# Performance work log

Measured on AMD Instinct MI355X. Metric: run time of the kernel, lower is better.

## Reference

```python
import jax, jax.numpy as jnp
import numpy as np

N, S, D, H, E, ETYPES = 1024, 64, 256, 4, 4096, 4
HD = D // H
EPS = 1e-5


def setup_inputs() -> dict:
    key = jax.random.key(0)
    ks = jax.random.split(key, 8)
    node_features = jax.random.normal(ks[0], (N, S, D), dtype=jnp.float32)
    lengths = jax.random.randint(ks[1], (N,), 1, S + 1)
    node_masks = (jnp.arange(S)[None, :] < lengths[:, None]).astype(jnp.float32)
    # unique edges (torch builds an adjacency matrix, so duplicates collapse)
    rng = np.random.default_rng(0)
    cand = rng.integers(0, N, size=(4 * E, 2))
    uniq = np.unique(cand, axis=0)
    assert uniq.shape[0] >= E
    perm = rng.permutation(uniq.shape[0])[:E]
    edge_index = jnp.asarray(uniq[perm].T, dtype=jnp.int64)  # [2, E]
    edge_type = jnp.asarray(rng.integers(1, ETYPES + 1, size=(E,)), dtype=jnp.int64)
    scale = 0.02
    wq = jax.random.normal(ks[2], (D, D), jnp.float32) * scale
    wk = jax.random.normal(ks[3], (D, D), jnp.float32) * scale
    wv = jax.random.normal(ks[4], (D, D), jnp.float32) * scale
    wo = jax.random.normal(ks[5], (D, D), jnp.float32) * scale
    return dict(
        node_features=node_features, node_masks=node_masks,
        ln_w=jnp.ones((D,), jnp.float32), ln_b=jnp.zeros((D,), jnp.float32),
        wq=wq, bq=jnp.zeros((D,), jnp.float32),
        wk=wk, bk=jnp.zeros((D,), jnp.float32),
        wv=wv, bv=jnp.zeros((D,), jnp.float32),
        wo=wo, bo=jnp.zeros((D,), jnp.float32),
        edge_type_weights=jnp.ones((ETYPES,), jnp.float32),
        edge_index=edge_index, edge_type=edge_type,
    )


def reference(node_features, node_masks, ln_w, ln_b, wq, bq, wk, bk, wv, bv,
              wo, bo, edge_type_weights, edge_index, edge_type):
    n, s, d = node_features.shape
    # LayerNorm (biased variance, eps=1e-5, as torch)
    mu = jnp.mean(node_features, axis=-1, keepdims=True)
    var = jnp.mean((node_features - mu) ** 2, axis=-1, keepdims=True)
    xn = (node_features - mu) * jax.lax.rsqrt(var + EPS) * ln_w + ln_b
    q = (xn @ wq + bq).reshape(n, s, H, HD)
    k = (xn @ wk + bk).reshape(n, s, H, HD)
    v = (xn @ wv + bv).reshape(n, s, H, HD)
    src, dst = edge_index[0], edge_index[1]
    # per-edge scalar bias: softplus(edge_type_weights[type-1]).clamp(1e-6, 1e6)
    ew = jnp.clip(jax.nn.softplus(edge_type_weights[edge_type - 1]), 1e-6, 1e6)  # [E]
    qe, ke, ve = q[src], k[dst], v[dst]              # [E,S,H,HD]
    km = node_masks[dst]                              # [E,S] key-side mask
    qm = node_masks[src]                              # [E,S] query-side mask
    scores = jnp.einsum('eqhd,ekhd->ehqk', qe, ke) / jnp.sqrt(jnp.float32(HD))
    scores = scores + ew[:, None, None, None]
    neg = jnp.float32(-1e30)
    scores = jnp.where(km[:, None, None, :] > 0, scores, neg)
    # per-edge softmax over the key node's valid tokens; zero rows where no valid key
    attn = jax.nn.softmax(scores, axis=-1) * km[:, None, None, :]
    ctx = jnp.einsum('ehqk,ekhd->eqhd', attn, ve) * qm[:, :, None, None]  # [E,S,H,HD]
    out = jax.ops.segment_sum(ctx, src, num_segments=n)   # sum over incident edges
    out = out.reshape(n, s, d)
    out = out @ wo + bo                                   # output projection (dropout=eval noop)
    out = out + node_features                             # residual
    return out * node_masks[..., None]
```

## Files before the change

kernel.cpp:

```cpp
#include <hip/hip_runtime.h>

#define DDIM 256
#define NEDGE 4096
#define SLEN 64
#define NNODE 1024
#define ROWS 65536

typedef short s16x8 __attribute__((ext_vector_type(8)));
typedef float f32x4 __attribute__((ext_vector_type(4)));

static __device__ __forceinline__ unsigned short f2bf(float f){
  union { float f; unsigned u; } v; v.f = f;
  unsigned r = v.u + 0x7FFFu + ((v.u >> 16) & 1u);
  return (unsigned short)(r >> 16);
}

static __device__ __forceinline__ void gl2lds16(const unsigned short* g, unsigned short* l){
  __builtin_amdgcn_global_load_lds((const __attribute__((address_space(1))) unsigned int*)g,
                                   (__attribute__((address_space(3))) unsigned int*)l, 16, 0, 0);
}

__global__ __launch_bounds__(256) void setup_kernel(const float* nf, const float* lnw, const float* lnb,
                                                    const float* wq, const float* wk, const float* wv, const float* wo,
                                                    const float* bq, const float* bk, const float* bv,
                                                    const float* masks, const int* eidx,
                                                    unsigned short* xn, unsigned short* Wqkv, unsigned short* Wo_t,
                                                    float* qkvb, int* lenp, int* deg){
  int bid = blockIdx.x, tid = threadIdx.x;
  if (bid < 16384){
    int lane = tid & 63;
    int row = bid*4 + (tid >> 6);
    const float4 x4 = ((const float4*)(nf + (size_t)row*DDIM))[lane];
    float s  = x4.x + x4.y + x4.z + x4.w;
    float sq = x4.x*x4.x + x4.y*x4.y + x4.z*x4.z + x4.w*x4.w;
    for (int off=1; off<64; off<<=1){ s += __shfl_xor(s, off); sq += __shfl_xor(sq, off); }
    float mu  = s  * (1.0f/DDIM);
    float var = sq * (1.0f/DDIM) - mu*mu;
    float rs  = rsqrtf(var + 1e-5f);
    float4 w4 = ((const float4*)lnw)[lane];
    float4 b4 = ((const float4*)lnb)[lane];
    ushort4 o;
    o.x = f2bf((x4.x - mu)*rs*w4.x + b4.x);
    o.y = f2bf((x4.y - mu)*rs*w4.y + b4.y);
    o.z = f2bf((x4.z - mu)*rs*w4.z + b4.z);
    o.w = f2bf((x4.w - mu)*rs*w4.w + b4.w);
    ((ushort4*)(xn + (size_t)row*DDIM))[lane] = o;
  } else if (bid < 17412){
    int idx = (bid - 16384)*256 + tid;
    if (idx < 196608){
      int mat = idx >> 16;
      int rem = idx & 65535;
      int n = rem >> 8, k = rem & 255;
      const float* W = (mat==0)?wq:(mat==1)?wk:wv;
      Wqkv[(size_t)(mat*256 + n)*256 + k] = f2bf(W[k*256 + n]);
    } else if (idx < 262144){
      int rem = idx - 196608;
      int n = rem >> 8, k = rem & 255;
      Wo_t[(size_t)n*256 + k] = f2bf(wo[k*256 + n]);
    } else if (idx < 262912){
      int i = idx - 262144;
      qkvb[i] = (i < 256) ? bq[i] : (i < 512) ? bk[i-256] : bv[i-512];
    }
  } else if (bid < 17668){
    int lane = tid & 63;
    int node = (bid - 17412)*4 + (tid >> 6);
    unsigned long long b = __ballot(masks[node*SLEN + lane] > 0.f);
    if (lane == 0) lenp[node] = __popcll(b);
  } else {
    int e = (bid - 17668)*256 + tid;
    if (e < NEDGE) atomicAdd(&deg[eidx[e]], 1);
  }
}

__global__ void scan_kernel(const int* deg, int* startp, int* order){
  __shared__ int buf[NNODE];
  __shared__ int hist[65];
  int t = threadIdx.x;
  int d = deg[t];
  buf[t] = d;
  if (t < 65) hist[t] = 0;
  __syncthreads();
  for (int off=1; off<NNODE; off<<=1){
    int v = (t >= off) ? buf[t-off] : 0;
    __syncthreads();
    buf[t] += v;
    __syncthreads();
  }
  startp[t] = buf[t] - d;
  int dc = d > 64 ? 64 : d;
  atomicAdd(&hist[dc], 1);
  __syncthreads();
  if (t == 0){
    int acc = 0;
    for (int i = 64; i >= 0; i--){ int h = hist[i]; hist[i] = acc; acc += h; }
  }
  __syncthreads();
  int pos = atomicAdd(&hist[dc], 1);
  order[pos] = t;
}

__global__ __launch_bounds__(256) void edge_fill_kernel(const int* eidx, const int* startp, int* cursor, int* elist){
  int e = blockIdx.x*256 + threadIdx.x;
  if (e < NEDGE){
    int s = eidx[e];
    int p = atomicAdd(&cursor[s], 1);
    elist[startp[s] + p] = eidx[NEDGE + e];
  }
}

__global__ __launch_bounds__(256) void qkv_kernel(const unsigned short* xn, const unsigned short* Wqkv,
                                                  const float* qkvb,
                                                  unsigned short* qb, unsigned short* kb_, unsigned short* vt){
  __shared__ __align__(16) unsigned short As[4096];
  __shared__ __align__(16) unsigned short Bs[8192];
  int tid = threadIdx.x;
  int lane = tid & 63, wid = tid >> 6, m = lane & 15, quad = lane >> 4;
  int row0 = blockIdx.x * 64;
  int col0 = blockIdx.y * 128;
  int rw = (wid & 1) * 32, cw = (wid >> 1) * 64;
  f32x4 acc[8];
  #pragma unroll
  for (int i=0;i<8;i++) acc[i] = (f32x4){0.f,0.f,0.f,0.f};
  for (int kc = 0; kc < 4; kc++){
    __syncthreads();
    #pragma unroll
    for (int i=0;i<2;i++){
      int cid = i*256 + tid, row = cid >> 3, c8 = cid & 7;
      gl2lds16(xn + (size_t)(row0 + row)*DDIM + kc*64 + ((c8 ^ (row&7))<<3), As + cid*8);
    }
    #pragma unroll
    for (int i=0;i<4;i++){
      int cid = i*256 + tid, row = cid >> 3, c8 = cid & 7;
      gl2lds16(Wqkv + (size_t)(col0 + row)*DDIM + kc*64 + ((c8 ^ (row&7))<<3), Bs + cid*8);
    }
    __syncthreads();
    #pragma unroll
    for (int ks=0; ks<2; ks++){
      int sw = ((ks*4 + quad) ^ (m&7)) << 3;
      s16x8 af[2], bf[4];
      #pragma unroll
      for (int mt=0;mt<2;mt++) af[mt] = *(const s16x8*)(As + (rw + mt*16 + m)*64 + sw);
      #pragma unroll
      for (int nt=0;nt<4;nt++) bf[nt] = *(const s16x8*)(Bs + (cw + nt*16 + m)*64 + sw);
      #pragma unroll
      for (int mt=0;mt<2;mt++)
        #pragma unroll
        for (int nt=0;nt<4;nt++)
          acc[mt*4+nt] = __builtin_amdgcn_mfma_f32_16x16x32_bf16(af[mt], bf[nt], acc[mt*4+nt], 0,0,0);
    }
  }
  int node = row0 >> 6;
  #pragma unroll
  for (int nt=0;nt<4;nt++){
    int cg = col0 + cw + nt*16 + m;
    int mat = cg >> 8, col = cg & 255;
    float bb = qkvb[cg];
    if (mat < 2){
      unsigned short* ob = (mat==0)?qb:kb_;
      #pragma unroll
      for (int mt=0;mt<2;mt++)
        #pragma unroll
        for (int r=0;r<4;r++){
          int row = row0 + rw + mt*16 + quad*4 + r;
          ob[(size_t)row*DDIM + col] = f2bf(acc[mt*4+nt][r] + bb);
        }
    } else {
      #pragma unroll
      for (int mt=0;mt<2;mt++){
        int tok0 = rw + mt*16 + quad*4;
        ushort4 p;
        p.x = f2bf(acc[mt*4+nt][0] + bb);
        p.y = f2bf(acc[mt*4+nt][1] + bb);
        p.z = f2bf(acc[mt*4+nt][2] + bb);
        p.w = f2bf(acc[mt*4+nt][3] + bb);
        *(ushort4*)(vt + ((size_t)node*256 + col)*64 + tok0) = p;
      }
    }
  }
}

__global__ __launch_bounds__(256) void attn_kernel(const unsigned short* qb, const unsigned short* kbuf,
                                                   const unsigned short* vtb, const int* lenp,
                                                   const int* startp, const int* degp, const int* elist,
                                                   const int* order, unsigned short* ctxb){
  __shared__ __align__(16) unsigned short Kt[2][4096];
  __shared__ __align__(16) unsigned short Vt[2][4096];
  __shared__ unsigned short P[4096];
  int tid = threadIdx.x;
  int lane = tid & 63, wid = tid >> 6, m = lane & 15, quad = lane >> 4;
  int src = order[blockIdx.x], h = blockIdx.y;
  int ls = lenp[src];
  int qtm = (ls + 15) >> 4;
  int s0 = startp[src], dg = degp[src];
  bool active = wid < qtm;
  unsigned short* Pw = P + wid*1024;

  s16x8 qf0 = {0,0,0,0,0,0,0,0}, qf1 = {0,0,0,0,0,0,0,0};
  if (active){
    const unsigned short* qbase = qb + (size_t)(src*SLEN + wid*16 + m)*DDIM + h*64 + quad*8;
    qf0 = *(const s16x8*)(qbase);
    qf1 = *(const s16x8*)(qbase + 32);
  }
  f32x4 o[4];
  #pragma unroll
  for (int i=0;i<4;i++) o[i] = (f32x4){0.f,0.f,0.f,0.f};

  int dst0 = 0, dst1 = 0, ld0 = 0;
  if (dg > 0){
    dst0 = elist[s0];
    ld0 = lenp[dst0];
    int kch = ((ld0 + 15) >> 4) * 128;
    #pragma unroll
    for (int i=0;i<2;i++){
      int cid = i*256 + tid;
      if (i*256 + wid*64 < kch){
        int row = cid >> 3, c8 = cid & 7;
        gl2lds16(kbuf + (size_t)(dst0*SLEN + row)*DDIM + h*64 + ((c8 ^ (row&7))<<3), Kt[0] + cid*8);
      }
    }
    const unsigned short* vhead = vtb + ((size_t)dst0*256 + h*64)*64;
    #pragma unroll
    for (int i=0;i<2;i++){
      int cid = i*256 + tid, row = cid >> 3, c8 = cid & 7;
      gl2lds16(vhead + row*64 + ((c8 ^ (row&7))<<3), Vt[0] + cid*8);
    }
  }
  if (dg > 1) dst1 = elist[s0 + 1];
  __syncthreads();

  for (int ei=0; ei<dg; ei++){
    int cur = ei & 1, nxt = cur ^ 1;
    int dst2 = (ei+2 < dg) ? elist[s0 + ei + 2] : 0;
    int ld1 = 0;
    if (ei+1 < dg){
      ld1 = lenp[dst1];
      int kch = ((ld1 + 15) >> 4) * 128;
      #pragma unroll
      for (int i=0;i<2;i++){
        int cid = i*256 + tid;
        if (i*256 + wid*64 < kch){
          int row = cid >> 3, c8 = cid & 7;
          gl2lds16(kbuf + (size_t)(dst1*SLEN + row)*DDIM + h*64 + ((c8 ^ (row&7))<<3), Kt[nxt] + cid*8);
        }
      }
      const unsigned short* vhead = vtb + ((size_t)dst1*256 + h*64)*64;
      #pragma unroll
      for (int i=0;i<2;i++){
        int cid = i*256 + tid, row = cid >> 3, c8 = cid & 7;
        gl2lds16(vhead + row*64 + ((c8 ^ (row&7))<<3), Vt[nxt] + cid*8);
      }
    }
    int ktm = (ld0 + 15) >> 4;
    int ks2 = (ktm + 1) >> 1;
    if (active){
      f32x4 acc[4];
      #pragma unroll
      for (int i=0;i<4;i++) acc[i] = (f32x4){0.f,0.f,0.f,0.f};
      #pragma unroll
      for (int kt=0; kt<4; kt++) if (kt < ktm){
        int key = kt*16 + m;
        s16x8 b0 = *(const s16x8*)(Kt[cur] + key*64 + ((quad ^ (m&7))<<3));
        acc[kt] = __builtin_amdgcn_mfma_f32_16x16x32_bf16(qf0, b0, acc[kt], 0,0,0);
        s16x8 b1 = *(const s16x8*)(Kt[cur] + key*64 + (((4 + quad) ^ (m&7))<<3));
        acc[kt] = __builtin_amdgcn_mfma_f32_16x16x32_bf16(qf1, b1, acc[kt], 0,0,0);
      }
      #pragma unroll
      for (int r=0; r<4; r++){
        float x[4];
        #pragma unroll
        for (int kt=0; kt<4; kt++)
          x[kt] = (kt < ktm && kt*16 + m < ld0) ? __expf(acc[kt][r]*0.125f) : 0.f;
        float s = x[0] + x[1] + x[2] + x[3];
        for (int off=1; off<16; off<<=1) s += __shfl_xor(s, off);
        float inv = 1.0f / s;
        int q = quad*4 + r;
        #pragma unroll
        for (int kt=0; kt<4; kt++) if (kt < 2*ks2){
          int key = kt*16 + m;
          Pw[q*64 + (((key>>3)^(q&7))<<3) + (key&7)] = f2bf(x[kt]*inv);
        }
      }
      #pragma unroll
      for (int ks=0; ks<2; ks++) if (ks < ks2){
        s16x8 pa = *(const s16x8*)(Pw + m*64 + ((((ks*4+quad))^(m&7))<<3));
        #pragma unroll
        for (int dt=0; dt<4; dt++){
          int d = dt*16 + m;
          s16x8 vf = *(const s16x8*)(Vt[cur] + d*64 + (((ks*4+quad)^(d&7))<<3));
          o[dt] = __builtin_amdgcn_mfma_f32_16x16x32_bf16(pa, vf, o[dt], 0,0,0);
        }
      }
    }
    dst0 = dst1; ld0 = ld1; dst1 = dst2;
    __syncthreads();
  }
  if (active){
    #pragma unroll
    for (int dt=0; dt<4; dt++){
      int col = h*64 + dt*16 + m;
      #pragma unroll
      for (int r=0; r<4; r++){
        int row = src*SLEN + wid*16 + quad*4 + r;
        ctxb[(size_t)row*DDIM + col] = f2bf(o[dt][r]);
      }
    }
  }
}

__global__ __launch_bounds__(256) void out_kernel(const unsigned short* ctxb, const unsigned short* Wo_t,
                                                  const float* bo, const float* nf, const float* masks,
                                                  float* out){
  __shared__ __align__(16) unsigned short As[4096];
  __shared__ __align__(16) unsigned short Bs[8192];
  int tid = threadIdx.x;
  int lane = tid & 63, wid = tid >> 6, m = lane & 15, quad = lane >> 4;
  int row0 = blockIdx.x * 64;
  int col0 = blockIdx.y * 128;
  int rw = (wid & 1) * 32, cw = (wid >> 1) * 64;
  f32x4 acc[8];
  #pragma unroll
  for (int i=0;i<8;i++) acc[i] = (f32x4){0.f,0.f,0.f,0.f};
  for (int kc = 0; kc < 4; kc++){
    __syncthreads();
    #pragma unroll
    for (int i=0;i<2;i++){
      int cid = i*256 + tid, row = cid >> 3, c8 = cid & 7;
      gl2lds16(ctxb + (size_t)(row0 + row)*DDIM + kc*64 + ((c8 ^ (row&7))<<3), As + cid*8);
    }
    #pragma unroll
    for (int i=0;i<4;i++){
      int cid = i*256 + tid, row = cid >> 3, c8 = cid & 7;
      gl2lds16(Wo_t + (size_t)(col0 + row)*DDIM + kc*64 + ((c8 ^ (row&7))<<3), Bs + cid*8);
    }
    __syncthreads();
    #pragma unroll
    for (int ks=0; ks<2; ks++){
      int sw = ((ks*4 + quad) ^ (m&7)) << 3;
      s16x8 af[2], bf[4];
      #pragma unroll
      for (int mt=0;mt<2;mt++) af[mt] = *(const s16x8*)(As + (rw + mt*16 + m)*64 + sw);
      #pragma unroll
      for (int nt=0;nt<4;nt++) bf[nt] = *(const s16x8*)(Bs + (cw + nt*16 + m)*64 + sw);
      #pragma unroll
      for (int mt=0;mt<2;mt++)
        #pragma unroll
        for (int nt=0;nt<4;nt++)
          acc[mt*4+nt] = __builtin_amdgcn_mfma_f32_16x16x32_bf16(af[mt], bf[nt], acc[mt*4+nt], 0,0,0);
    }
  }
  #pragma unroll
  for (int nt=0;nt<4;nt++){
    int col = col0 + cw + nt*16 + m;
    float bb = bo[col];
    #pragma unroll
    for (int mt=0;mt<2;mt++)
      #pragma unroll
      for (int r=0;r<4;r++){
        int row = row0 + rw + mt*16 + quad*4 + r;
        float v = acc[mt*4+nt][r] + bb + nf[(size_t)row*DDIM + col];
        out[(size_t)row*DDIM + col] = v * masks[row];
      }
  }
}

extern "C" void kernel_launch(void* const* d_in, const int* in_sizes, int n_in,
                              void* d_out, int out_size, void* d_ws, size_t ws_size,
                              hipStream_t stream){
  const float* nf    = (const float*)d_in[0];
  const float* masks = (const float*)d_in[1];
  const float* lnw   = (const float*)d_in[2];
  const float* lnb   = (const float*)d_in[3];
  const float* wq    = (const float*)d_in[4];
  const float* bq    = (const float*)d_in[5];
  const float* wk    = (const float*)d_in[6];
  const float* bk    = (const float*)d_in[7];
  const float* wv    = (const float*)d_in[8];
  const float* bv    = (const float*)d_in[9];
  const float* wo    = (const float*)d_in[10];
  const float* bo    = (const float*)d_in[11];
  const int*   eidx  = (const int*)d_in[13];
  float* out = (float*)d_out;

  char* ws = (char*)d_ws;
  const size_t B = (size_t)ROWS * DDIM * 2;
  unsigned short* xn   = (unsigned short*)(ws);
  unsigned short* qb   = (unsigned short*)(ws + B);
  unsigned short* kb   = (unsigned short*)(ws + 2*B);
  unsigned short* vt   = (unsigned short*)(ws + 3*B);
  unsigned short* ctxb = (unsigned short*)(ws + 4*B);
  char* wp = ws + 5*B;
  unsigned short* Wqkv = (unsigned short*)(wp);
  unsigned short* Wo_t = (unsigned short*)(wp + 393216);
  float* qkvb         = (float*)(wp + 524288);
  char* ip = wp + 528384;
  int* deg    = (int*)(ip);
  int* cursor = (int*)(ip + 4096);
  int* startp = (int*)(ip + 8192);
  int* lenp   = (int*)(ip + 12288);
  int* order  = (int*)(ip + 16384);
  int* elist  = (int*)(ip + 20480);

  hipMemsetAsync(deg, 0, 8192, stream);
  setup_kernel<<<17684, 256, 0, stream>>>(nf, lnw, lnb, wq, wk, wv, wo, bq, bk, bv,
                                          masks, eidx, xn, Wqkv, Wo_t, qkvb, lenp, deg);
  scan_kernel<<<1, NNODE, 0, stream>>>(deg, startp, order);
  edge_fill_kernel<<<NEDGE/256, 256, 0, stream>>>(eidx, startp, cursor, elist);
  qkv_kernel<<<dim3(ROWS/64, 6), 256, 0, stream>>>(xn, Wqkv, qkvb, qb, kb, vt);
  attn_kernel<<<dim3(NNODE, 4), 256, 0, stream>>>(qb, kb, vt, lenp, startp, deg, elist, order, ctxb);
  out_kernel<<<dim3(ROWS/64, 2), 256, 0, stream>>>(ctxb, Wo_t, bo, nf, masks, out);
}
```

Baseline: 352.0 us.

## Merge CSR build into one kernel and skip padded token tiles in GEMMs

The memset, degree atomics, scan and edge-fill kernels are folded into a single 1024-thread CSR kernel that counts degrees and fills edge lists with shared-memory atomics, removing two launches and a memset. The QKV and output projection GEMMs now read each node's valid length and skip loading, MFMA work and stores for 16-row tiles beyond the padded length. In the output kernel those rows are written as zeros directly. The CSR step now runs on a single block, which puts it on the serial path.

Result: no change. 345.7 us (-1.8%).

```diff
diff --git a/kernel.cpp b/kernel.cpp
--- a/kernel.cpp
+++ b/kernel.cpp
@@ -23,9 +23,9 @@
 __global__ __launch_bounds__(256) void setup_kernel(const float* nf, const float* lnw, const float* lnb,
                                                     const float* wq, const float* wk, const float* wv, const float* wo,
                                                     const float* bq, const float* bk, const float* bv,
-                                                    const float* masks, const int* eidx,
+                                                    const float* masks,
                                                     unsigned short* xn, unsigned short* Wqkv, unsigned short* Wo_t,
-                                                    float* qkvb, int* lenp, int* deg){
+                                                    float* qkvb, int* lenp){
   int bid = blockIdx.x, tid = threadIdx.x;
   if (bid < 16384){
     int lane = tid & 63;
@@ -61,24 +61,28 @@
       int i = idx - 262144;
       qkvb[i] = (i < 256) ? bq[i] : (i < 512) ? bk[i-256] : bv[i-512];
     }
-  } else if (bid < 17668){
+  } else {
     int lane = tid & 63;
     int node = (bid - 17412)*4 + (tid >> 6);
     unsigned long long b = __ballot(masks[node*SLEN + lane] > 0.f);
     if (lane == 0) lenp[node] = __popcll(b);
-  } else {
-    int e = (bid - 17668)*256 + tid;
-    if (e < NEDGE) atomicAdd(&deg[eidx[e]], 1);
-  }
-}
-
-__global__ void scan_kernel(const int* deg, int* startp, int* order){
+  }
+}
+
+__global__ void csr_kernel(const int* eidx, int* startp, int* order, int* degp, int* elist){
+  __shared__ int deg[NNODE];
   __shared__ int buf[NNODE];
   __shared__ int hist[65];
+  __shared__ int cur[NNODE];
   int t = threadIdx.x;
+  deg[t] = 0;
+  if (t < 65) hist[t] = 0;
+  __syncthreads();
+  #pragma unroll
+  for (int i=0;i<4;i++) atomicAdd(&deg[eidx[i*1024 + t]], 1);
+  __syncthreads();
   int d = deg[t];
   buf[t] = d;
-  if (t < 65) hist[t] = 0;
   __syncthreads();
   for (int off=1; off<NNODE; off<<=1){
     int v = (t >= off) ? buf[t-off] : 0;
@@ -86,38 +90,42 @@
     buf[t] += v;
     __syncthreads();
   }
-  startp[t] = buf[t] - d;
+  int st = buf[t] - d;
+  startp[t] = st; degp[t] = d; cur[t] = st;
   int dc = d > 64 ? 64 : d;
   atomicAdd(&hist[dc], 1);
   __syncthreads();
   if (t == 0){
     int acc = 0;
-    for (int i = 64; i >= 0; i--){ int h = hist[i]; hist[i] = acc; acc += h; }
+    for (int i=64;i>=0;i--){ int h = hist[i]; hist[i] = acc; acc += h; }
   }
   __syncthreads();
   int pos = atomicAdd(&hist[dc], 1);
   order[pos] = t;
-}
-
-__global__ __launch_bounds__(256) void edge_fill_kernel(const int* eidx, const int* startp, int* cursor, int* elist){
-  int e = blockIdx.x*256 + threadIdx.x;
-  if (e < NEDGE){
+  __syncthreads();
+  #pragma unroll
+  for (int i=0;i<4;i++){
+    int e = i*1024 + t;
     int s = eidx[e];
-    int p = atomicAdd(&cursor[s], 1);
-    elist[startp[s] + p] = eidx[NEDGE + e];
+    int p = atomicAdd(&cur[s], 1);
+    elist[p] = eidx[NEDGE + e];
   }
 }
 
 __global__ __launch_bounds__(256) void qkv_kernel(const unsigned short* xn, const unsigned short* Wqkv,
-                                                  const float* qkvb,
+                                                  const float* qkvb, const int* lenp,
                                                   unsigned short* qb, unsigned short* kb_, unsigned short* vt){
   __shared__ __align__(16) unsigned short As[4096];
   __shared__ __align__(16) unsigned short Bs[8192];
   int tid = threadIdx.x;
   int lane = tid & 63, wid = tid >> 6, m = lane & 15, quad = lane >> 4;
   int row0 = blockIdx.x * 64;
+  int node = row0 >> 6;
+  int qtm = (lenp[node] + 15) >> 4;
+  int vrows = qtm << 4;
   int col0 = blockIdx.y * 128;
   int rw = (wid & 1) * 32, cw = (wid >> 1) * 64;
+  int t0 = rw >> 4;
   f32x4 acc[8];
   #pragma unroll
   for (int i=0;i<8;i++) acc[i] = (f32x4){0.f,0.f,0.f,0.f};
@@ -125,8 +133,10 @@
     __syncthreads();
     #pragma unroll
     for (int i=0;i<2;i++){
-      int cid = i*256 + tid, row = cid >> 3, c8 = cid & 7;
-      gl2lds16(xn + (size_t)(row0 + row)*DDIM + kc*64 + ((c8 ^ (row&7))<<3), As + cid*8);
+      if (i*32 + wid*8 < vrows){
+        int cid = i*256 + tid, row = cid >> 3, c8 = cid & 7;
+        gl2lds16(xn + (size_t)(row0 + row)*DDIM + kc*64 + ((c8 ^ (row&7))<<3), As + cid*8);
+      }
     }
     #pragma unroll
     for (int i=0;i<4;i++){
@@ -139,17 +149,16 @@
       int sw = ((ks*4 + quad) ^ (m&7)) << 3;
       s16x8 af[2], bf[4];
       #pragma unroll
-      for (int mt=0;mt<2;mt++) af[mt] = *(const s16x8*)(As + (rw + mt*16 + m)*64 + sw);
+      for (int mt=0;mt<2;mt++) if (t0 + mt < qtm) af[mt] = *(const s16x8*)(As + (rw + mt*16 + m)*64 + sw);
       #pragma unroll
       for (int nt=0;nt<4;nt++) bf[nt] = *(const s16x8*)(Bs + (cw + nt*16 + m)*64 + sw);
       #pragma unroll
-      for (int mt=0;mt<2;mt++)
+      for (int mt=0;mt<2;mt++) if (t0 + mt < qtm)
         #pragma unroll
         for (int nt=0;nt<4;nt++)
           acc[mt*4+nt] = __builtin_amdgcn_mfma_f32_16x16x32_bf16(af[mt], bf[nt], acc[mt*4+nt], 0,0,0);
     }
   }
-  int node = row0 >> 6;
   #pragma unroll
   for (int nt=0;nt<4;nt++){
     int cg = col0 + cw + nt*16 + m;
@@ -158,7 +167,7 @@
     if (mat < 2){
       unsigned short* ob = (mat==0)?qb:kb_;
       #pragma unroll
-      for (int mt=0;mt<2;mt++)
+      for (int mt=0;mt<2;mt++) if (t0 + mt < qtm)
         #pragma unroll
         for (int r=0;r<4;r++){
           int row = row0 + rw + mt*16 + quad*4 + r;
@@ -166,7 +175,7 @@
         }
     } else {
       #pragma unroll
-      for (int mt=0;mt<2;mt++){
+      for (int mt=0;mt<2;mt++) if (t0 + mt < qtm){
         int tok0 = rw + mt*16 + quad*4;
         ushort4 p;
         p.x = f2bf(acc[mt*4+nt][0] + bb);
@@ -309,14 +318,18 @@
 
 __global__ __launch_bounds__(256) void out_kernel(const unsigned short* ctxb, const unsigned short* Wo_t,
                                                   const float* bo, const float* nf, const float* masks,
-                                                  float* out){
+                                                  const int* lenp, float* out){
   __shared__ __align__(16) unsigned short As[4096];
   __shared__ __align__(16) unsigned short Bs[8192];
   int tid = threadIdx.x;
   int lane = tid & 63, wid = tid >> 6, m = lane & 15, quad = lane >> 4;
   int row0 = blockIdx.x * 64;
+  int node = row0 >> 6;
+  int qtm = (lenp[node] + 15) >> 4;
+  int vrows = qtm << 4;
   int col0 = blockIdx.y * 128;
   int rw = (wid & 1) * 32, cw = (wid >> 1) * 64;
+  int t0 = rw >> 4;
   f32x4 acc[8];
   #pragma unroll
   for (int i=0;i<8;i++) acc[i] = (f32x4){0.f,0.f,0.f,0.f};
@@ -324,8 +337,10 @@
     __syncthreads();
     #pragma unroll
     for (int i=0;i<2;i++){
-      int cid = i*256 + tid, row = cid >> 3, c8 = cid & 7;
-      gl2lds16(ctxb + (size_t)(row0 + row)*DDIM + kc*64 + ((c8 ^ (row&7))<<3), As + cid*8);
+      if (i*32 + wid*8 < vrows){
+        int cid = i*256 + tid, row = cid >> 3, c8 = cid & 7;
+        gl2lds16(ctxb + (size_t)(row0 + row)*DDIM + kc*64 + ((c8 ^ (row&7))<<3), As + cid*8);
+      }
     }
     #pragma unroll
     for (int i=0;i<4;i++){
@@ -338,11 +353,11 @@
       int sw = ((ks*4 + quad) ^ (m&7)) << 3;
       s16x8 af[2], bf[4];
       #pragma unroll
-      for (int mt=0;mt<2;mt++) af[mt] = *(const s16x8*)(As + (rw + mt*16 + m)*64 + sw);
+      for (int mt=0;mt<2;mt++) if (t0 + mt < qtm) af[mt] = *(const s16x8*)(As + (rw + mt*16 + m)*64 + sw);
       #pragma unroll
       for (int nt=0;nt<4;nt++) bf[nt] = *(const s16x8*)(Bs + (cw + nt*16 + m)*64 + sw);
       #pragma unroll
-      for (int mt=0;mt<2;mt++)
+      for (int mt=0;mt<2;mt++) if (t0 + mt < qtm)
         #pragma unroll
         for (int nt=0;nt<4;nt++)
           acc[mt*4+nt] = __builtin_amdgcn_mfma_f32_16x16x32_bf16(af[mt], bf[nt], acc[mt*4+nt], 0,0,0);
@@ -353,13 +368,22 @@
     int col = col0 + cw + nt*16 + m;
     float bb = bo[col];
     #pragma unroll
-    for (int mt=0;mt<2;mt++)
-      #pragma unroll
-      for (int r=0;r<4;r++){
-        int row = row0 + rw + mt*16 + quad*4 + r;
-        float v = acc[mt*4+nt][r] + bb + nf[(size_t)row*DDIM + col];
-        out[(size_t)row*DDIM + col] = v * masks[row];
-      }
+    for (int mt=0;mt<2;mt++){
+      if (t0 + mt < qtm){
+        #pragma unroll
+        for (int r=0;r<4;r++){
+          int row = row0 + rw + mt*16 + quad*4 + r;
+          float v = acc[mt*4+nt][r] + bb + nf[(size_t)row*DDIM + col];
+          out[(size_t)row*DDIM + col] = v * masks[row];
+        }
+      } else {
+        #pragma unroll
+        for (int r=0;r<4;r++){
+          int row = row0 + rw + mt*16 + quad*4 + r;
+          out[(size_t)row*DDIM + col] = 0.f;
+        }
+      }
+    }
   }
 }
 
@@ -393,19 +417,16 @@
   unsigned short* Wo_t = (unsigned short*)(wp + 393216);
   float* qkvb         = (float*)(wp + 524288);
   char* ip = wp + 528384;
-  int* deg    = (int*)(ip);
-  int* cursor = (int*)(ip + 4096);
-  int* startp = (int*)(ip + 8192);
-  int* lenp   = (int*)(ip + 12288);
-  int* order  = (int*)(ip + 16384);
-  int* elist  = (int*)(ip + 20480);
-
-  hipMemsetAsync(deg, 0, 8192, stream);
-  setup_kernel<<<17684, 256, 0, stream>>>(nf, lnw, lnb, wq, wk, wv, wo, bq, bk, bv,
-                                          masks, eidx, xn, Wqkv, Wo_t, qkvb, lenp, deg);
-  scan_kernel<<<1, NNODE, 0, stream>>>(deg, startp, order);
-  edge_fill_kernel<<<NEDGE/256, 256, 0, stream>>>(eidx, startp, cursor, elist);
-  qkv_kernel<<<dim3(ROWS/64, 6), 256, 0, stream>>>(xn, Wqkv, qkvb, qb, kb, vt);
-  attn_kernel<<<dim3(NNODE, 4), 256, 0, stream>>>(qb, kb, vt, lenp, startp, deg, elist, order, ctxb);
-  out_kernel<<<dim3(ROWS/64, 2), 256, 0, stream>>>(ctxb, Wo_t, bo, nf, masks, out);
-}
+  int* startp = (int*)(ip);
+  int* lenp   = (int*)(ip + 4096);
+  int* order  = (int*)(ip + 8192);
+  int* degp   = (int*)(ip + 12288);
+  int* elist  = (int*)(ip + 16384);
+
+  setup_kernel<<<17668, 256, 0, stream>>>(nf, lnw, lnb, wq, wk, wv, wo, bq, bk, bv,
+                                          masks, xn, Wqkv, Wo_t, qkvb, lenp);
+  csr_kernel<<<1, 1024, 0, stream>>>(eidx, startp, order, degp, elist);
+  qkv_kernel<<<dim3(ROWS/64, 6), 256, 0, stream>>>(xn, Wqkv, qkvb, lenp, qb, kb, vt);
+  attn_kernel<<<dim3(NNODE, 4), 256, 0, stream>>>(qb, kb, vt, lenp, startp, degp, elist, order, ctxb);
+  out_kernel<<<dim3(ROWS/64, 2), 256, 0, stream>>>(ctxb, Wo_t, bo, nf, masks, lenp, out);
+}
```
